# Kernel tuning notes

Hardware: AMD Instinct MI355X
Metric: run time of the kernel (lower is better)

Reference implementation:

```python
import jax, jax.numpy as jnp
import numpy as np
import math

B, T, D, H = 4, 2048, 2048, 16
HD = D // H  # 128


def rotate_half(x):
    half = x.shape[-1] // 2
    return jnp.concatenate([-x[..., half:], x[..., :half]], axis=-1)


def apply_rope(x, cos, sin):
    # x: [B,H,T,hd]; cos/sin: [T,hd] -> broadcast over B,H
    return x * cos[None, None] + rotate_half(x) * sin[None, None]


def setup_inputs() -> dict:
    key = jax.random.key(0)
    ks = jax.random.split(key, 6)
    x = jax.random.normal(ks[0], (B, T, D), dtype=jnp.float32)
    # standard RoPE tables
    inv_freq = 1.0 / (10000.0 ** (np.arange(0, HD, 2, dtype=np.float32) / HD))
    freqs = np.arange(T, dtype=np.float32)[:, None] * inv_freq[None, :]  # [T, hd/2]
    emb = np.concatenate([freqs, freqs], axis=-1)  # [T, hd]
    cos = jnp.asarray(np.cos(emb))
    sin = jnp.asarray(np.sin(emb))
    # additive causal mask [T,T]: 0 on/below diagonal, -1e9 above
    mask = jnp.where(jnp.tril(jnp.ones((T, T), dtype=bool)), 0.0, -1e9).astype(jnp.float32)
    scale = 0.02
    Wq = scale * jax.random.normal(ks[1], (D, D), dtype=jnp.float32)
    Wk = scale * jax.random.normal(ks[2], (D, D), dtype=jnp.float32)
    Wv = scale * jax.random.normal(ks[3], (D, D), dtype=jnp.float32)
    Wo = scale * jax.random.normal(ks[4], (D, D), dtype=jnp.float32)
    return {"x": x, "cos": cos, "sin": sin, "mask": mask,
            "Wq": Wq, "Wk": Wk, "Wv": Wv, "Wo": Wo}


def reference(x, cos, sin, mask, Wq, Wk, Wv, Wo):
    b, t, d = x.shape

    def split_heads(y):  # [B,T,D] -> [B,H,T,hd]
        return y.reshape(b, t, H, HD).transpose(0, 2, 1, 3)

    # nn.Linear: y = x @ W.T
    Q = apply_rope(split_heads(jnp.einsum('btd,od->bto', x, Wq)), cos, sin)
    K = apply_rope(split_heads(jnp.einsum('btd,od->bto', x, Wk)), cos, sin)
    V = split_heads(jnp.einsum('btd,od->bto', x, Wv))

    scores = jnp.einsum('bhqd,bhkd->bhqk', Q, K) / math.sqrt(HD)
    scores = scores + mask  # [T,T] broadcasts over [B,H,T,T]
    weights = jax.nn.softmax(scores, axis=-1)
    out = jnp.einsum('bhqk,bhkd->bhqd', weights, V)
    out = out.transpose(0, 2, 1, 3).reshape(b, t, d)
    return jnp.einsum('btd,od->bto', out, Wo)
```

## Files before the change

kernel.cpp:

```cpp
#include <hip/hip_runtime.h>
#include <hip/hip_bf16.h>

#define DEV static __device__ __forceinline__

typedef __attribute__((ext_vector_type(8))) _Float16 half8;
typedef __attribute__((ext_vector_type(4))) float f32x4;

constexpr int Bc = 4, Tc = 2048, Dc = 2048, Hc = 16;

DEV ushort f2h(float f) { _Float16 h = (_Float16)f; return __builtin_bit_cast(ushort, h); }
DEV float  h2f(ushort u) { return (float)__builtin_bit_cast(_Float16, u); }
DEV uint pk2h(float a, float b) {
  return __builtin_bit_cast(uint, __builtin_amdgcn_cvt_pkrtz(a, b));
}

DEV f32x4 MFMA(half8 a, half8 b, f32x4 c) {
  return __builtin_amdgcn_mfma_f32_16x16x32_f16(a, b, c, 0, 0, 0);
}

DEV void async_cp16(void* lds, const void* g) {
  __builtin_amdgcn_global_load_lds((const __attribute__((address_space(1))) void*)g,
                                   (__attribute__((address_space(3))) void*)lds,
                                   16, 0, 0);
}

__global__ __launch_bounds__(256) void cvt(const float* __restrict__ in,
                                           ushort* __restrict__ out, int n4) {
  const int i = blockIdx.x * 256 + threadIdx.x;
  if (i >= n4) return;
  const float4 v = ((const float4*)in)[i];
  ushort4 o;
  o.x = f2h(v.x); o.y = f2h(v.y); o.z = f2h(v.z); o.w = f2h(v.w);
  ((ushort4*)out)[i] = o;
}

template <typename OutT>
__global__ __launch_bounds__(512, 2) void gemm256(const ushort* __restrict__ A,
                                                  const ushort* __restrict__ Bw,
                                                  OutT* __restrict__ C) {
  __shared__ ushort As[4][256 * 32];
  __shared__ ushort Bs[4][256 * 32];
  const int tid = threadIdx.x;
  const int lane = tid & 63, wid = tid >> 6;
  const int g = lane >> 4, q16 = lane & 15;
  const int wm = wid >> 2, wn = wid & 3;

  const int flat = (int)blockIdx.x;
  const int xcd = flat & 7, idx = flat >> 3;
  const int bm = xcd * 4 + (idx & 3);
  const int bn = idx >> 2;
  const ushort* Ab = A + (size_t)bm * 256 * Dc;
  const ushort* Bb = Bw + (size_t)bn * 256 * Dc;

#define STAGE1(KT, BUF, PH) do {                                               \
    const int pass_ = (PH) & 1;                                                \
    const int c_ = pass_ * 512 + tid;                                          \
    const int row_ = c_ >> 2, gl_ = c_ & 3;                                    \
    const int col_ = (KT) * 32 + ((gl_ ^ ((row_ >> 1) & 3)) << 3);             \
    if ((PH) < 2)                                                              \
      async_cp16(&As[BUF][(pass_ * 512 + wid * 64) * 8],                       \
                 Ab + (size_t)row_ * Dc + col_);                               \
    else                                                                       \
      async_cp16(&Bs[BUF][(pass_ * 512 + wid * 64) * 8],                       \
                 Bb + (size_t)row_ * Dc + col_);                               \
  } while (0)

  f32x4 acc[8][4] = {};

  for (int tt = 0; tt < 3; ++tt) {
    STAGE1(tt, tt, 0); STAGE1(tt, tt, 1);
    STAGE1(tt, tt, 2); STAGE1(tt, tt, 3);
  }

  const int sgz = (g ^ ((q16 >> 1) & 3)) << 3;

#pragma unroll 1
  for (int t = 0; t < 64; ++t) {
    const int rb = t & 3;
    const int sb = (t + 3) & 3;
    const bool st = (t + 3) < 64;
    const ushort* Asb = As[rb];
    const ushort* Bsb = Bs[rb];

    if (t + 2 < 64)      asm volatile("s_waitcnt vmcnt(8)" ::: "memory");
    else if (t + 1 < 64) asm volatile("s_waitcnt vmcnt(4)" ::: "memory");
    else                 asm volatile("s_waitcnt vmcnt(0)" ::: "memory");
    __builtin_amdgcn_s_barrier();
    __builtin_amdgcn_sched_barrier(0);

    half8 af0[4], af1[4], bf[4];
#pragma unroll
    for (int nf = 0; nf < 4; ++nf) {
      const int r = wn * 64 + nf * 16 + q16;
      bf[nf] = *(const half8*)&Bsb[r * 32 + sgz];
    }
#pragma unroll
    for (int mf = 0; mf < 4; ++mf) {
      const int r = wm * 128 + mf * 16 + q16;
      af0[mf] = *(const half8*)&Asb[r * 32 + sgz];
    }
#pragma unroll
    for (int mf = 0; mf < 4; ++mf) {
      const int r = wm * 128 + 64 + mf * 16 + q16;
      af1[mf] = *(const half8*)&Asb[r * 32 + sgz];
    }
    if (st) { STAGE1(t + 3, sb, 0); STAGE1(t + 3, sb, 1);
              STAGE1(t + 3, sb, 2); STAGE1(t + 3, sb, 3); }

    __builtin_amdgcn_s_setprio(1);
#pragma unroll
    for (int mf = 0; mf < 4; ++mf)
#pragma unroll
      for (int nf = 0; nf < 4; ++nf)
        acc[mf][nf] = MFMA(af0[mf], bf[nf], acc[mf][nf]);
#pragma unroll
    for (int mf = 0; mf < 4; ++mf)
#pragma unroll
      for (int nf = 0; nf < 4; ++nf)
        acc[4 + mf][nf] = MFMA(af1[mf], bf[nf], acc[4 + mf][nf]);
    __builtin_amdgcn_s_setprio(0);
  }
#undef STAGE1

  const int m00 = bm * 256 + wm * 128 + g * 4;
  const int n0 = bn * 256 + wn * 64 + q16;
#pragma unroll
  for (int mf = 0; mf < 8; ++mf)
#pragma unroll
    for (int nf = 0; nf < 4; ++nf) {
      const int m0 = m00 + mf * 16;
      const int n = n0 + nf * 16;
#pragma unroll
      for (int r = 0; r < 4; ++r) {
        const float v = acc[mf][nf][r];
        if constexpr (sizeof(OutT) == 2)
          C[(size_t)(m0 + r) * Dc + n] = (OutT)f2h(v);
        else
          C[(size_t)(m0 + r) * Dc + n] = (OutT)v;
      }
    }
}

__global__ __launch_bounds__(256) void rope(ushort* __restrict__ X,
                                            const float* __restrict__ cs,
                                            const float* __restrict__ sn) {
  const int tid = blockIdx.x * 256 + threadIdx.x;
  const int row = tid >> 4;
  const int jq = (tid & 15) << 2;
  const int t = (row >> 4) & (Tc - 1);
  ushort* base = X + (size_t)row * 128;
  const ushort4 lo = *(const ushort4*)(base + jq);
  const ushort4 hi = *(const ushort4*)(base + 64 + jq);
  const float4 c4 = *(const float4*)(cs + t * 128 + jq);
  const float4 s4 = *(const float4*)(sn + t * 128 + jq);
  const float xl[4] = {h2f(lo.x), h2f(lo.y), h2f(lo.z), h2f(lo.w)};
  const float xh[4] = {h2f(hi.x), h2f(hi.y), h2f(hi.z), h2f(hi.w)};
  const float cc[4] = {c4.x, c4.y, c4.z, c4.w};
  const float ss[4] = {s4.x, s4.y, s4.z, s4.w};
  ushort4 olo, ohi;
  ushort* po = (ushort*)&olo;
  ushort* ph = (ushort*)&ohi;
#pragma unroll
  for (int k = 0; k < 4; ++k) {
    po[k] = f2h(xl[k] * cc[k] - xh[k] * ss[k]);
    ph[k] = f2h(xh[k] * cc[k] + xl[k] * ss[k]);
  }
  *(ushort4*)(base + jq) = olo;
  *(ushort4*)(base + 64 + jq) = ohi;
}

__global__ __launch_bounds__(512, 2) void attn(const ushort* __restrict__ Q,
                                               const ushort* __restrict__ K,
                                               const ushort* __restrict__ V,
                                               ushort* __restrict__ O) {
  __shared__ ushort Ks[2][64 * 128];
  __shared__ ushort Vt[2][128 * 64];

  const int tid = threadIdx.x;
  const int lane = tid & 63, wid = tid >> 6;
  const int g = lane >> 4, q16 = lane & 15;

  const int flat = (int)(blockIdx.x + 4 * blockIdx.y);
  const int xcd = flat & 7, idx = flat >> 3;
  const int bh = xcd + 8 * (idx & 7);
  const int pr = idx >> 3;

  const int b = bh >> 4, h = bh & 15;
  const size_t headbase = ((size_t)b * Tc * Hc + h) * 128;
  const float SCL2 = 0.12751743f;

  const int vdc = (wid & 3) * 4 + (lane & 3);
  const int vkvp = (wid >> 2) * 16 + (lane >> 2);

  uint4 vreg[2];

#define ISSUEK(KT, BUF) do {                                                   \
    const ushort* Kb_ = K + headbase + (size_t)(KT) * 64 * Dc;                 \
    _Pragma("unroll") for (int i_ = 0; i_ < 2; ++i_) {                         \
      const int c_ = i_ * 512 + tid;                                           \
      const int kv_ = c_ >> 4, gl_ = c_ & 15;                                  \
      async_cp16(&Ks[BUF][(i_ * 512 + wid * 64) * 8],                          \
                 Kb_ + (size_t)kv_ * Dc + ((gl_ ^ (kv_ & 7)) << 3));           \
    }                                                                          \
  } while (0)

#define LOADV(KT) do {                                                         \
    const ushort* p0_ = V + headbase + (size_t)((KT) * 64 + 2 * vkvp) * Dc +   \
                        vdc * 8;                                               \
    vreg[0] = *(const uint4*)p0_;                                              \
    vreg[1] = *(const uint4*)(p0_ + Dc);                                       \
  } while (0)

#define WRITEV(BUF) do {                                                       \
    const ushort* e0_ = (const ushort*)&vreg[0];                               \
    const ushort* e1_ = (const ushort*)&vreg[1];                               \
    _Pragma("unroll") for (int j_ = 0; j_ < 8; ++j_) {                         \
      const int d_ = vdc * 8 + j_;                                             \
      const unsigned w_ = (unsigned)e0_[j_] | ((unsigned)e1_[j_] << 16);       \
      *(unsigned*)&Vt[BUF][(d_ * 64 + 2 * vkvp) ^ ((d_ & 7) << 3)] = w_;       \
    }                                                                          \
  } while (0)

#pragma unroll 1
  for (int half = 0; half < 2; ++half) {
    const int q0 = (half ? pr : 7 - pr) * 256;
    const int qrow = q0 + wid * 32;
    const int nt = q0 / 64 + 4;

    half8 qreg[2][4];
#pragma unroll
    for (int qf = 0; qf < 2; ++qf)
#pragma unroll
      for (int ds = 0; ds < 4; ++ds)
        qreg[qf][ds] = *(const half8*)(Q + headbase +
                       (size_t)(qrow + qf * 16 + q16) * Dc + ds * 32 + g * 8);

    f32x4 oacc[2][8] = {};
    float m_[2] = {-1e30f, -1e30f};
    float l_[2] = {0.f, 0.f};

    __builtin_amdgcn_s_barrier();
    __builtin_amdgcn_sched_barrier(0);
    ISSUEK(0, 0);
    LOADV(0);
    WRITEV(0);

#pragma unroll 1
    for (int kt = 0; kt < nt; ++kt) {
      const int cur = kt & 1;
      const int kv0 = kt * 64;
      asm volatile("s_waitcnt vmcnt(0) lgkmcnt(0)" ::: "memory");
      __builtin_amdgcn_s_barrier();
      __builtin_amdgcn_sched_barrier(0);
      if (kt + 1 < nt) {
        ISSUEK(kt + 1, cur ^ 1);
        LOADV(kt + 1);
      }

      if (kv0 <= qrow + 31) {
        const ushort* Ksb = Ks[cur];
        const ushort* Vtb = Vt[cur];
        f32x4 s[2][4] = {};
        __builtin_amdgcn_s_setprio(1);
#pragma unroll
        for (int ds = 0; ds < 4; ++ds) {
          half8 kf[4];
#pragma unroll
          for (int kvf = 0; kvf < 4; ++kvf) {
            const int kv = kvf * 16 + q16;
            kf[kvf] = *(const half8*)&Ksb[(kv * 128 + ds * 32 + g * 8) ^ ((kv & 7) << 3)];
          }
#pragma unroll
          for (int kvf = 0; kvf < 4; ++kvf)
#pragma unroll
            for (int qf = 0; qf < 2; ++qf)
              s[qf][kvf] = MFMA(kf[kvf], qreg[qf][ds], s[qf][kvf]);
        }
        __builtin_amdgcn_s_setprio(0);
        float pmax[2] = {-1e30f, -1e30f};
        if (kv0 + 63 > qrow) {
#pragma unroll
          for (int qf = 0; qf < 2; ++qf) {
            const int qg = qrow + qf * 16 + q16;
#pragma unroll
            for (int kvf = 0; kvf < 4; ++kvf)
#pragma unroll
              for (int r = 0; r < 4; ++r) {
                float v = s[qf][kvf][r];
                if ((kv0 + kvf * 16 + g * 4 + r) > qg) v = -1e30f;
                s[qf][kvf][r] = v;
                pmax[qf] = fmaxf(pmax[qf], v);
              }
          }
        } else {
#pragma unroll
          for (int qf = 0; qf < 2; ++qf)
#pragma unroll
            for (int kvf = 0; kvf < 4; ++kvf)
#pragma unroll
              for (int r = 0; r < 4; ++r)
                pmax[qf] = fmaxf(pmax[qf], s[qf][kvf][r]);
        }
#pragma unroll
        for (int qf = 0; qf < 2; ++qf) {
          pmax[qf] = fmaxf(pmax[qf], __shfl_xor(pmax[qf], 16));
          pmax[qf] = fmaxf(pmax[qf], __shfl_xor(pmax[qf], 32));
        }
        if (!__all((pmax[0] <= m_[0] + 16.f) & (pmax[1] <= m_[1] + 16.f))) {
#pragma unroll
          for (int qf = 0; qf < 2; ++qf) {
            const float mn2 = fmaxf(m_[qf], pmax[qf]);
            const float alpha = __builtin_exp2f((m_[qf] - mn2) * SCL2);
            m_[qf] = mn2;
            l_[qf] *= alpha;
#pragma unroll
            for (int df = 0; df < 8; ++df)
              oacc[qf][df] *= alpha;
          }
        }
        uint w[2][4][2];
#pragma unroll
        for (int qf = 0; qf < 2; ++qf) {
          const float mn = m_[qf];
          float lsum = 0.f;
#pragma unroll
          for (int kvf = 0; kvf < 4; ++kvf) {
            const float p0 = __builtin_exp2f((s[qf][kvf][0] - mn) * SCL2);
            const float p1 = __builtin_exp2f((s[qf][kvf][1] - mn) * SCL2);
            const float p2 = __builtin_exp2f((s[qf][kvf][2] - mn) * SCL2);
            const float p3 = __builtin_exp2f((s[qf][kvf][3] - mn) * SCL2);
            lsum += (p0 + p1) + (p2 + p3);
            w[qf][kvf][0] = pk2h(p0, p1);
            w[qf][kvf][1] = pk2h(p2, p3);
          }
          l_[qf] += lsum;
        }
        const bool ghi = g >= 2;
        const bool godd = (g & 1) != 0;
        half8 pb[2][2];
#pragma unroll
        for (int qf = 0; qf < 2; ++qf) {
          uint sA[2][2], sB[2][2];
#pragma unroll
          for (int c = 0; c < 2; ++c)
#pragma unroll
            for (int i = 0; i < 2; ++i) {
              sA[c][i] = ghi ? w[qf][2 * c + 1][i] : w[qf][2 * c][i];
              sB[c][i] = ghi ? w[qf][2 * c][i] : w[qf][2 * c + 1][i];
            }
          uint x16[2][2], x32[2][2], x48[2][2];
#pragma unroll
          for (int c = 0; c < 2; ++c)
#pragma unroll
            for (int i = 0; i < 2; ++i) {
              x16[c][i] = __shfl_xor(sA[c][i], 16);
              x32[c][i] = __shfl_xor(sB[c][i], 32);
              x48[c][i] = __shfl_xor(sB[c][i], 48);
            }
#pragma unroll
          for (int c = 0; c < 2; ++c) {
            uint4 t;
            t.x = godd ? (ghi ? x16[c][0] : x48[c][0]) : (ghi ? x32[c][0] : sA[c][0]);
            t.y = godd ? (ghi ? x16[c][1] : x48[c][1]) : (ghi ? x32[c][1] : sA[c][1]);
            t.z = godd ? (ghi ? sA[c][0] : x32[c][0]) : (ghi ? x48[c][0] : x16[c][0]);
            t.w = godd ? (ghi ? sA[c][1] : x32[c][1]) : (ghi ? x48[c][1] : x16[c][1]);
            pb[qf][c] = __builtin_bit_cast(half8, t);
          }
        }
        __builtin_amdgcn_s_setprio(1);
#pragma unroll
        for (int c = 0; c < 2; ++c) {
#pragma unroll
          for (int df = 0; df < 8; ++df) {
            const int d = df * 16 + q16;
            const half8 vf = *(const half8*)&Vtb[(d * 64 + c * 32 + g * 8) ^ ((d & 7) << 3)];
#pragma unroll
            for (int qf = 0; qf < 2; ++qf)
              oacc[qf][df] = MFMA(vf, pb[qf][c], oacc[qf][df]);
          }
        }
        __builtin_amdgcn_s_setprio(0);
      }

      if (kt + 1 < nt) WRITEV(cur ^ 1);
    }

#pragma unroll
    for (int qf = 0; qf < 2; ++qf) {
      float l = l_[qf];
      l += __shfl_xor(l, 16);
      l += __shfl_xor(l, 32);
      const float inv = 1.0f / l;
      const int t = qrow + qf * 16 + q16;
#pragma unroll
      for (int df = 0; df < 8; ++df) {
        const f32x4 v = oacc[qf][df];
        ushort4 o;
        o.x = f2h(v[0] * inv); o.y = f2h(v[1] * inv);
        o.z = f2h(v[2] * inv); o.w = f2h(v[3] * inv);
        *(ushort4*)(O + headbase + (size_t)t * Dc + df * 16 + g * 4) = o;
      }
    }
  }
#undef ISSUEK
#undef LOADV
#undef WRITEV
}

extern "C" void kernel_launch(void* const* d_in, const int* in_sizes, int n_in,
                              void* d_out, int out_size, void* d_ws, size_t ws_size,
                              hipStream_t stream) {
  (void)in_sizes; (void)n_in; (void)out_size; (void)ws_size;
  const float* x  = (const float*)d_in[0];
  const float* cs = (const float*)d_in[1];
  const float* sn = (const float*)d_in[2];
  const float* Wq = (const float*)d_in[4];
  const float* Wk = (const float*)d_in[5];
  const float* Wv = (const float*)d_in[6];
  const float* Wo = (const float*)d_in[7];
  float* out = (float*)d_out;

  char* ws = (char*)d_ws;
  const size_t MB = 1024 * 1024;
  ushort* xb  = (ushort*)(ws);
  ushort* wqb = (ushort*)(ws + 32 * MB);
  ushort* wkb = (ushort*)(ws + 40 * MB);
  ushort* wvb = (ushort*)(ws + 48 * MB);
  ushort* wob = (ushort*)(ws + 56 * MB);
  ushort* Qr  = (ushort*)(ws + 64 * MB);
  ushort* Kr  = (ushort*)(ws + 96 * MB);
  ushort* Vr  = (ushort*)(ws + 128 * MB);

  cvt<<<16384, 256, 0, stream>>>(x, xb, 4194304);
  cvt<<<4096, 256, 0, stream>>>(Wq, wqb, 1048576);
  cvt<<<4096, 256, 0, stream>>>(Wk, wkb, 1048576);
  cvt<<<4096, 256, 0, stream>>>(Wv, wvb, 1048576);
  cvt<<<4096, 256, 0, stream>>>(Wo, wob, 1048576);

  gemm256<ushort><<<256, 512, 0, stream>>>(xb, wqb, Qr);
  gemm256<ushort><<<256, 512, 0, stream>>>(xb, wkb, Kr);
  gemm256<ushort><<<256, 512, 0, stream>>>(xb, wvb, Vr);

  rope<<<8192, 256, 0, stream>>>(Qr, cs, sn);
  rope<<<8192, 256, 0, stream>>>(Kr, cs, sn);

  attn<<<dim3(4, 64), 512, 0, stream>>>(Qr, Kr, Vr, xb);

  gemm256<float><<<256, 512, 0, stream>>>(xb, wob, out);
}
```

Before: 471.6 us.

## Fuse QKV projections into one GEMM launch with RoPE in the epilogue

Wq and Wk rows are permuted during conversion so that each rotate-half pair lands in the same warp's accumulator fragments. A single 768-block GEMM then computes Q, K and V together, relying on the weight buffers being contiguous in the workspace, and applies RoPE in the epilogue for the Q and K tiles. This removes two rope kernels, the extra read and write of Q and K they caused, and two GEMM launches. In exchange the epilogue does scattered cos/sin loads, and correctness depends on the contiguous workspace layout and the index permutation.

Measured after the change: 456.4 us. 1.03x faster.

```diff
diff --git a/kernel.cpp b/kernel.cpp
--- a/kernel.cpp
+++ b/kernel.cpp
@@ -34,10 +34,24 @@
   ((ushort4*)out)[i] = o;
 }
 
-template <typename OutT>
-__global__ __launch_bounds__(512, 2) void gemm256(const ushort* __restrict__ A,
+__global__ __launch_bounds__(256) void wcvt_rope(const float* __restrict__ in,
+                                                 ushort* __restrict__ out) {
+  const int i = blockIdx.x * 256 + threadIdx.x;
+  const int row = i >> 9, cidx = i & 511;
+  const int h = row >> 7, fr = row & 127;
+  const int s_ = fr >> 6, j = fr & 63;
+  const int rowp = h * 128 + (j >> 4) * 32 + s_ * 16 + (j & 15);
+  const float4 v = ((const float4*)in)[i];
+  ushort4 o;
+  o.x = f2h(v.x); o.y = f2h(v.y); o.z = f2h(v.z); o.w = f2h(v.w);
+  ((ushort4*)(out))[rowp * 512 + cidx] = o;
+}
+
+__global__ __launch_bounds__(512, 2) void gemmqkv(const ushort* __restrict__ A,
                                                   const ushort* __restrict__ Bw,
-                                                  OutT* __restrict__ C) {
+                                                  ushort* __restrict__ Cq,
+                                                  const float* __restrict__ cs,
+                                                  const float* __restrict__ sn) {
   __shared__ ushort As[4][256 * 32];
   __shared__ ushort Bs[4][256 * 32];
   const int tid = threadIdx.x;
@@ -122,6 +136,131 @@
   }
 #undef STAGE1
 
+  ushort* C = Cq + (size_t)(bn >> 3) * ((size_t)8192 * Dc);
+  const int bn8 = bn & 7;
+  const int m00 = bm * 256 + wm * 128 + g * 4;
+  const int n0 = bn8 * 256 + wn * 64 + q16;
+
+  if (bn < 16) {
+#pragma unroll
+    for (int mf = 0; mf < 8; ++mf)
+#pragma unroll
+      for (int p = 0; p < 2; ++p) {
+        const int j = ((wn & 1) * 2 + p) * 16 + q16;
+#pragma unroll
+        for (int r = 0; r < 4; ++r) {
+          const int m = m00 + mf * 16 + r;
+          const int t = m & (Tc - 1);
+          const float c = cs[t * 128 + j];
+          const float s_ = sn[t * 128 + j];
+          const float lo = acc[mf][2 * p][r];
+          const float hi = acc[mf][2 * p + 1][r];
+          C[(size_t)m * Dc + n0 + (2 * p) * 16] = f2h(lo * c - hi * s_);
+          C[(size_t)m * Dc + n0 + (2 * p + 1) * 16] = f2h(hi * c + lo * s_);
+        }
+      }
+  } else {
+#pragma unroll
+    for (int mf = 0; mf < 8; ++mf)
+#pragma unroll
+      for (int nf = 0; nf < 4; ++nf) {
+        const int m0 = m00 + mf * 16;
+        const int n = n0 + nf * 16;
+#pragma unroll
+        for (int r = 0; r < 4; ++r)
+          C[(size_t)(m0 + r) * Dc + n] = f2h(acc[mf][nf][r]);
+      }
+  }
+}
+
+template <typename OutT>
+__global__ __launch_bounds__(512, 2) void gemm256(const ushort* __restrict__ A,
+                                                  const ushort* __restrict__ Bw,
+                                                  OutT* __restrict__ C) {
+  __shared__ ushort As[4][256 * 32];
+  __shared__ ushort Bs[4][256 * 32];
+  const int tid = threadIdx.x;
+  const int lane = tid & 63, wid = tid >> 6;
+  const int g = lane >> 4, q16 = lane & 15;
+  const int wm = wid >> 2, wn = wid & 3;
+
+  const int flat = (int)blockIdx.x;
+  const int xcd = flat & 7, idx = flat >> 3;
+  const int bm = xcd * 4 + (idx & 3);
+  const int bn = idx >> 2;
+  const ushort* Ab = A + (size_t)bm * 256 * Dc;
+  const ushort* Bb = Bw + (size_t)bn * 256 * Dc;
+
+#define STAGE1(KT, BUF, PH) do {                                               \
+    const int pass_ = (PH) & 1;                                                \
+    const int c_ = pass_ * 512 + tid;                                          \
+    const int row_ = c_ >> 2, gl_ = c_ & 3;                                    \
+    const int col_ = (KT) * 32 + ((gl_ ^ ((row_ >> 1) & 3)) << 3);             \
+    if ((PH) < 2)                                                              \
+      async_cp16(&As[BUF][(pass_ * 512 + wid * 64) * 8],                       \
+                 Ab + (size_t)row_ * Dc + col_);                               \
+    else                                                                       \
+      async_cp16(&Bs[BUF][(pass_ * 512 + wid * 64) * 8],                       \
+                 Bb + (size_t)row_ * Dc + col_);                               \
+  } while (0)
+
+  f32x4 acc[8][4] = {};
+
+  for (int tt = 0; tt < 3; ++tt) {
+    STAGE1(tt, tt, 0); STAGE1(tt, tt, 1);
+    STAGE1(tt, tt, 2); STAGE1(tt, tt, 3);
+  }
+
+  const int sgz = (g ^ ((q16 >> 1) & 3)) << 3;
+
+#pragma unroll 1
+  for (int t = 0; t < 64; ++t) {
+    const int rb = t & 3;
+    const int sb = (t + 3) & 3;
+    const bool st = (t + 3) < 64;
+    const ushort* Asb = As[rb];
+    const ushort* Bsb = Bs[rb];
+
+    if (t + 2 < 64)      asm volatile("s_waitcnt vmcnt(8)" ::: "memory");
+    else if (t + 1 < 64) asm volatile("s_waitcnt vmcnt(4)" ::: "memory");
+    else                 asm volatile("s_waitcnt vmcnt(0)" ::: "memory");
+    __builtin_amdgcn_s_barrier();
+    __builtin_amdgcn_sched_barrier(0);
+
+    half8 af0[4], af1[4], bf[4];
+#pragma unroll
+    for (int nf = 0; nf < 4; ++nf) {
+      const int r = wn * 64 + nf * 16 + q16;
+      bf[nf] = *(const half8*)&Bsb[r * 32 + sgz];
+    }
+#pragma unroll
+    for (int mf = 0; mf < 4; ++mf) {
+      const int r = wm * 128 + mf * 16 + q16;
+      af0[mf] = *(const half8*)&Asb[r * 32 + sgz];
+    }
+#pragma unroll
+    for (int mf = 0; mf < 4; ++mf) {
+      const int r = wm * 128 + 64 + mf * 16 + q16;
+      af1[mf] = *(const half8*)&Asb[r * 32 + sgz];
+    }
+    if (st) { STAGE1(t + 3, sb, 0); STAGE1(t + 3, sb, 1);
+              STAGE1(t + 3, sb, 2); STAGE1(t + 3, sb, 3); }
+
+    __builtin_amdgcn_s_setprio(1);
+#pragma unroll
+    for (int mf = 0; mf < 4; ++mf)
+#pragma unroll
+      for (int nf = 0; nf < 4; ++nf)
+        acc[mf][nf] = MFMA(af0[mf], bf[nf], acc[mf][nf]);
+#pragma unroll
+    for (int mf = 0; mf < 4; ++mf)
+#pragma unroll
+      for (int nf = 0; nf < 4; ++nf)
+        acc[4 + mf][nf] = MFMA(af1[mf], bf[nf], acc[4 + mf][nf]);
+    __builtin_amdgcn_s_setprio(0);
+  }
+#undef STAGE1
+
   const int m00 = bm * 256 + wm * 128 + g * 4;
   const int n0 = bn * 256 + wn * 64 + q16;
 #pragma unroll
@@ -139,34 +278,6 @@
           C[(size_t)(m0 + r) * Dc + n] = (OutT)v;
       }
     }
-}
-
-__global__ __launch_bounds__(256) void rope(ushort* __restrict__ X,
-                                            const float* __restrict__ cs,
-                                            const float* __restrict__ sn) {
-  const int tid = blockIdx.x * 256 + threadIdx.x;
-  const int row = tid >> 4;
-  const int jq = (tid & 15) << 2;
-  const int t = (row >> 4) & (Tc - 1);
-  ushort* base = X + (size_t)row * 128;
-  const ushort4 lo = *(const ushort4*)(base + jq);
-  const ushort4 hi = *(const ushort4*)(base + 64 + jq);
-  const float4 c4 = *(const float4*)(cs + t * 128 + jq);
-  const float4 s4 = *(const float4*)(sn + t * 128 + jq);
-  const float xl[4] = {h2f(lo.x), h2f(lo.y), h2f(lo.z), h2f(lo.w)};
-  const float xh[4] = {h2f(hi.x), h2f(hi.y), h2f(hi.z), h2f(hi.w)};
-  const float cc[4] = {c4.x, c4.y, c4.z, c4.w};
-  const float ss[4] = {s4.x, s4.y, s4.z, s4.w};
-  ushort4 olo, ohi;
-  ushort* po = (ushort*)&olo;
-  ushort* ph = (ushort*)&ohi;
-#pragma unroll
-  for (int k = 0; k < 4; ++k) {
-    po[k] = f2h(xl[k] * cc[k] - xh[k] * ss[k]);
-    ph[k] = f2h(xh[k] * cc[k] + xl[k] * ss[k]);
-  }
-  *(ushort4*)(base + jq) = olo;
-  *(ushort4*)(base + 64 + jq) = ohi;
 }
 
 __global__ __launch_bounds__(512, 2) void attn(const ushort* __restrict__ Q,
@@ -432,17 +543,12 @@
   ushort* Vr  = (ushort*)(ws + 128 * MB);
 
   cvt<<<16384, 256, 0, stream>>>(x, xb, 4194304);
-  cvt<<<4096, 256, 0, stream>>>(Wq, wqb, 1048576);
-  cvt<<<4096, 256, 0, stream>>>(Wk, wkb, 1048576);
+  wcvt_rope<<<4096, 256, 0, stream>>>(Wq, wqb);
+  wcvt_rope<<<4096, 256, 0, stream>>>(Wk, wkb);
   cvt<<<4096, 256, 0, stream>>>(Wv, wvb, 1048576);
   cvt<<<4096, 256, 0, stream>>>(Wo, wob, 1048576);
 
-  gemm256<ushort><<<256, 512, 0, stream>>>(xb, wqb, Qr);
-  gemm256<ushort><<<256, 512, 0, stream>>>(xb, wkb, Kr);
-  gemm256<ushort><<<256, 512, 0, stream>>>(xb, wvb, Vr);
-
-  rope<<<8192, 256, 0, stream>>>(Qr, cs, sn);
-  rope<<<8192, 256, 0, stream>>>(Kr, cs, sn);
+  gemmqkv<<<768, 512, 0, stream>>>(xb, wqb, Qr, cs, sn);
 
   attn<<<dim3(4, 64), 512, 0, stream>>>(Qr, Kr, Vr, xb);
 
```
